# Optimization experiments

Hardware: AMD Instinct MI355X
Metric: run time of the kernel (lower is better)

Reference implementation:

```python
import jax, jax.numpy as jnp
import numpy as np

EMBED = 1024
HEADS = 16


def setup_inputs() -> dict:
    key = jax.random.key(0)
    ks = jax.random.split(key, 7)
    scale = 1.0 / np.sqrt(EMBED)
    x = jax.random.normal(ks[0], (4, 2048, EMBED), dtype=jnp.float32)
    Wq = jax.random.normal(ks[1], (EMBED, EMBED), dtype=jnp.float32) * scale
    bq = jax.random.normal(ks[2], (EMBED,), dtype=jnp.float32) * 0.01
    Wk = jax.random.normal(ks[3], (EMBED, EMBED), dtype=jnp.float32) * scale
    bk = jax.random.normal(ks[4], (EMBED,), dtype=jnp.float32) * 0.01
    Wv = jax.random.normal(ks[5], (EMBED, EMBED), dtype=jnp.float32) * scale
    bv = jax.random.normal(ks[6], (EMBED,), dtype=jnp.float32) * 0.01
    return {"x": x, "Wq": Wq, "bq": bq, "Wk": Wk, "bk": bk, "Wv": Wv, "bv": bv}


def reference(x, Wq, bq, Wk, bk, Wv, bv):
    b, s, n = x.shape
    h = HEADS
    d = n // h
    # torch nn.Linear: y = x @ W.T + b
    q = (jnp.einsum("bsn,mn->bsm", x, Wq) + bq).reshape(b, s, h, d).transpose(0, 2, 1, 3)
    k = (jnp.einsum("bsn,mn->bsm", x, Wk) + bk).reshape(b, s, h, d).transpose(0, 2, 1, 3)
    v = (jnp.einsum("bsn,mn->bsm", x, Wv) + bv).reshape(b, s, h, d).transpose(0, 2, 1, 3)
    # scores: [b, h, s_q, s_k]; fixed scale of 1/10 as in the source
    scores = jnp.einsum("bhqd,bhkd->bhqk", q, k) / 10.0
    # NOTE: softmax over dim=-2 (the QUERY axis), matching the source exactly
    attn = jax.nn.softmax(scores, axis=-2)
    out = jnp.einsum("bhqk,bhkd->bhqd", attn, v)
    return out.transpose(0, 2, 1, 3).reshape(b, s, n)
```

## Files before the change

kernel.cpp:

```cpp
#include <hip/hip_runtime.h>
#include <math.h>

#define SEQ    2048
#define EMBED  1024
#define HEADS  16
#define HDIM   64
#define BATCH  4
#define ROWS   (BATCH * SEQ)
#define BH     (BATCH * HEADS)

typedef _Float16 f16;
typedef __attribute__((ext_vector_type(2))) _Float16 f16x2;
typedef __attribute__((ext_vector_type(4))) _Float16 f16x4;
typedef __attribute__((ext_vector_type(8))) _Float16 f16x8;
typedef __attribute__((ext_vector_type(4)))  float   f32x4;
typedef __attribute__((ext_vector_type(16))) float   f32x16;

#define EXP2C 0.14426950408889634f

__device__ __forceinline__ void async16(void* l, const void* g) {
    __builtin_amdgcn_global_load_lds(
        (__attribute__((address_space(1))) void*)(uintptr_t)g,
        (__attribute__((address_space(3))) void*)(uint32_t)(uintptr_t)l,
        16, 0, 0);
}
__device__ __forceinline__ f32x4 mfma16(f16x8 a, f16x8 b, f32x4 c) {
    return __builtin_amdgcn_mfma_f32_16x16x32_f16(a, b, c, 0, 0, 0);
}
__device__ __forceinline__ f32x16 mfma32(f16x8 a, f16x8 b, f32x16 c) {
    return __builtin_amdgcn_mfma_f32_32x32x16_f16(a, b, c, 0, 0, 0);
}
__device__ __forceinline__ f32x16 zero16() {
    f32x16 z;
#pragma unroll
    for (int i = 0; i < 16; ++i) z[i] = 0.f;
    return z;
}
__device__ __forceinline__ f16x2 pk2(float a, float b) {
    union {
        __fp16 __attribute__((ext_vector_type(2))) h;
        f16x2 f;
    } u;
    u.h = __builtin_amdgcn_cvt_pkrtz(a, b);
    return u.f;
}
__device__ __forceinline__ int swz64(int row, int gran) {
    return row * 64 + ((gran ^ (row & 7)) << 3);
}

#define NX4 (ROWS * EMBED / 4)
#define NW4 (EMBED * EMBED / 4)
__global__ __launch_bounds__(256) void cvt_kernel(
    const float* __restrict__ x,
    const float* __restrict__ Wq, const float* __restrict__ Wk,
    const float* __restrict__ Wv,
    f16* __restrict__ xh, f16* __restrict__ Wh)
{
    int i = blockIdx.x * 256 + threadIdx.x;
    const float4* src; f16* dst; int j;
    if (i < NX4)              { src = (const float4*)x;  dst = xh;                j = i; }
    else if (i < NX4 + NW4)   { src = (const float4*)Wq; dst = Wh;                j = i - NX4; }
    else if (i < NX4 + 2*NW4) { src = (const float4*)Wk; dst = Wh + EMBED*EMBED;  j = i - NX4 - NW4; }
    else                      { src = (const float4*)Wv; dst = Wh + 2*EMBED*EMBED;j = i - NX4 - 2*NW4; }
    float4 v = src[j];
    f16x4 h;
    h[0] = (f16)v.x; h[1] = (f16)v.y; h[2] = (f16)v.z; h[3] = (f16)v.w;
    *(f16x4*)(dst + (size_t)j * 4) = h;
}

__global__ __launch_bounds__(256) void proj_kernel(
    const f16* __restrict__ A,
    const f16* __restrict__ W,
    const float* __restrict__ bq, const float* __restrict__ bk,
    const float* __restrict__ bv,
    f16* __restrict__ Qh, f16* __restrict__ Kh, f16* __restrict__ Vt)
{
    __shared__ f16 As[128 * 32];
    __shared__ f16 Bs[128 * 32];
    __shared__ f16 Ts[64 * 132];

    const int t = threadIdx.x, wv = t >> 6, lane = t & 63;
    const int lm = lane & 15, quad = lane >> 4;
    const int r0 = blockIdx.x * 128, c0 = blockIdx.y * 128;
    const int wm = wv & 1, wn = wv >> 1;

    const int srow = lane >> 2;
    const int sgr  = (lane & 3) ^ (srow & 3);
    const f16* gA = A + (size_t)(r0 + wv * 32 + srow) * EMBED + sgr * 8;
    const f16* gB = W + (size_t)(c0 + wv * 32 + srow) * EMBED + sgr * 8;
    f16* lA = As + wv * 1024;
    f16* lB = Bs + wv * 1024;

    f32x4 acc[4][4];
#pragma unroll
    for (int i = 0; i < 4; ++i)
#pragma unroll
        for (int j = 0; j < 4; ++j) acc[i][j] = (f32x4){0.f, 0.f, 0.f, 0.f};

    for (int kk = 0; kk < EMBED; kk += 32) {
        __syncthreads();
        async16(lA,        gA + kk);
        async16(lA + 512,  gA + (size_t)16 * EMBED + kk);
        async16(lB,        gB + kk);
        async16(lB + 512,  gB + (size_t)16 * EMBED + kk);
        __syncthreads();

        f16x8 af[4], bf[4];
#pragma unroll
        for (int i = 0; i < 4; ++i) {
            int row = wm * 64 + i * 16 + lm;
            af[i] = *(const f16x8*)&As[row * 32 + ((quad ^ (row & 3)) << 3)];
        }
#pragma unroll
        for (int i = 0; i < 4; ++i) {
            int row = wn * 64 + i * 16 + lm;
            bf[i] = *(const f16x8*)&Bs[row * 32 + ((quad ^ (row & 3)) << 3)];
        }
#pragma unroll
        for (int mi = 0; mi < 4; ++mi)
#pragma unroll
            for (int ni = 0; ni < 4; ++ni)
                acc[mi][ni] = mfma16(af[mi], bf[ni], acc[mi][ni]);
    }

    const int z = c0 >> 10;
    const float* bias = (z == 0) ? bq : (z == 1) ? bk : bv;
    const int b  = r0 >> 11;
    const int s0 = r0 & 2047;

    if (z < 2) {
        f16* O = (z == 0) ? Qh : Kh;
#pragma unroll
        for (int ni = 0; ni < 4; ++ni) {
            int cz = (c0 & 1023) + wn * 64 + ni * 16 + lm;
            float bb = bias[cz];
            int h = cz >> 6, d = cz & 63;
#pragma unroll
            for (int mi = 0; mi < 4; ++mi) {
                int s = s0 + wm * 64 + mi * 16 + quad * 4;
                size_t base = ((size_t)(b * HEADS + h) * SEQ + s) * HDIM + d;
#pragma unroll
                for (int r = 0; r < 4; ++r)
                    O[base + (size_t)r * HDIM] = (f16)(acc[mi][ni][r] + bb);
            }
        }
    } else {
#pragma unroll 1
        for (int hd = 0; hd < 2; ++hd) {
            __syncthreads();
            if (wn == hd) {
#pragma unroll
                for (int ni = 0; ni < 4; ++ni) {
                    int cz = (c0 & 1023) + wn * 64 + ni * 16 + lm;
                    float bb = bias[cz];
                    int dloc = ni * 16 + lm;
#pragma unroll
                    for (int mi = 0; mi < 4; ++mi) {
                        int sloc = wm * 64 + mi * 16 + quad * 4;
                        f16x4 pk;
#pragma unroll
                        for (int r = 0; r < 4; ++r) pk[r] = (f16)(acc[mi][ni][r] + bb);
                        *(f16x4*)&Ts[dloc * 132 + sloc] = pk;
                    }
                }
            }
            __syncthreads();
            int hout = ((c0 & 1023) >> 6) + hd;
            int dl = t >> 2, soff = (t & 3) * 32;
            size_t gbase = ((size_t)(b * HEADS + hout) * HDIM + dl) * SEQ + s0 + soff;
#pragma unroll
            for (int c = 0; c < 8; ++c) {
                f16x4 v = *(const f16x4*)&Ts[dl * 132 + soff + 4 * c];
                *(f16x4*)&Vt[gbase + 4 * c] = v;
            }
        }
    }
}

__global__ __launch_bounds__(256) void stats_kernel(
    const f16* __restrict__ Qh, const f16* __restrict__ Kh,
    f16* __restrict__ Vt)
{
    __shared__ f16 Kst[256 * 64];
    __shared__ f16 Qs[64 * 64];
    __shared__ f16 Ls[256];

    const int t = threadIdx.x, wv = t >> 6, lane = t & 63;
    const int lm = lane & 31, half = lane >> 5;
    const int bh = blockIdx.y, k0 = blockIdx.x * 256;
    const size_t base  = (size_t)bh * SEQ * HDIM;
    const size_t vbase = (size_t)bh * HDIM * SEQ;

    const int srow = lane >> 3;
    const int sgr  = (lane & 7) ^ (srow & 7);

#pragma unroll
    for (int i = 0; i < 8; ++i) {
        int rr = wv * 64 + 8 * i;
        async16(Kst + rr * 64,
                Kh + base + (size_t)(k0 + rr + srow) * 64 + sgr * 8);
    }
    __syncthreads();

    f16x8 Kf[2][4];
#pragma unroll
    for (int kt = 0; kt < 2; ++kt)
#pragma unroll
        for (int kg = 0; kg < 4; ++kg)
            Kf[kt][kg] = *(const f16x8*)&Kst[swz64(wv * 64 + kt * 32 + lm, 2 * kg + half)];

    float cs0 = 0.f, cs1 = 0.f;
    for (int q0 = 0; q0 < SEQ; q0 += 64) {
        __syncthreads();
#pragma unroll
        for (int i = 0; i < 2; ++i) {
            int rr = wv * 16 + 8 * i;
            async16(Qs + rr * 64,
                    Qh + base + (size_t)(q0 + rr + srow) * 64 + sgr * 8);
        }
        __syncthreads();
#pragma unroll
        for (int qt = 0; qt < 2; ++qt) {
            f16x8 Qf[4];
#pragma unroll
            for (int kg = 0; kg < 4; ++kg)
                Qf[kg] = *(const f16x8*)&Qs[swz64(qt * 32 + lm, 2 * kg + half)];
            f32x16 s0v = zero16(), s1v = zero16();
#pragma unroll
            for (int kg = 0; kg < 4; ++kg) {
                s0v = mfma32(Qf[kg], Kf[0][kg], s0v);
                s1v = mfma32(Qf[kg], Kf[1][kg], s1v);
            }
#pragma unroll
            for (int e = 0; e < 16; ++e) {
                cs0 += exp2f(s0v[e] * EXP2C);
                cs1 += exp2f(s1v[e] * EXP2C);
            }
        }
    }
    cs0 += __shfl_xor(cs0, 32, 64);
    cs1 += __shfl_xor(cs1, 32, 64);
    if (half == 0) {
        Ls[wv * 64 + lm]      = (f16)(64.0f / cs0);
        Ls[wv * 64 + 32 + lm] = (f16)(64.0f / cs1);
    }
    __syncthreads();

    {
        int dl = t >> 2, koff = (t & 3) * 64;
        size_t g = vbase + (size_t)dl * SEQ + k0 + koff;
#pragma unroll
        for (int c = 0; c < 8; ++c) {
            f16x8 v  = *(const f16x8*)&Vt[g + 8 * c];
            f16x8 lv = *(const f16x8*)&Ls[koff + 8 * c];
            v = v * lv;
            *(f16x8*)&Vt[g + 8 * c] = v;
        }
    }
}

__global__ __launch_bounds__(256) void out_kernel(
    const f16* __restrict__ Qh, const f16* __restrict__ Kh,
    const f16* __restrict__ Vt, float* __restrict__ out)
{
    __shared__ f16 Qs[256 * 64];
    __shared__ f16 Ks[64 * 64];
    __shared__ f16 Vs[64 * 64];

    const int t = threadIdx.x, wv = t >> 6, lane = t & 63;
    const int lm = lane & 31, half = lane >> 5;
    const int bh = blockIdx.y, q0 = blockIdx.x * 256;
    const int b = bh >> 4, h = bh & 15;
    const size_t base  = (size_t)bh * SEQ * HDIM;
    const size_t vbase = (size_t)bh * HDIM * SEQ;

    const int srow = lane >> 3;
    const int sgr  = (lane & 7) ^ (srow & 7);

#pragma unroll
    for (int i = 0; i < 8; ++i) {
        int rr = wv * 64 + 8 * i;
        async16(Qs + rr * 64,
                Qh + base + (size_t)(q0 + rr + srow) * 64 + sgr * 8);
    }
    __syncthreads();

    f16x8 Qf[2][4];
#pragma unroll
    for (int qt = 0; qt < 2; ++qt)
#pragma unroll
        for (int kg = 0; kg < 4; ++kg)
            Qf[qt][kg] = *(const f16x8*)&Qs[swz64(wv * 64 + qt * 32 + lm, 2 * kg + half)];

    f32x16 oacc[2][2];
#pragma unroll
    for (int i = 0; i < 2; ++i)
#pragma unroll
        for (int j = 0; j < 2; ++j) oacc[i][j] = zero16();

    f16* Pw = Qs + wv * 64 * 64;

    for (int k0 = 0; k0 < SEQ; k0 += 64) {
        __syncthreads();
#pragma unroll
        for (int i = 0; i < 2; ++i) {
            int rr = wv * 16 + 8 * i;
            async16(Ks + rr * 64,
                    Kh + base + (size_t)(k0 + rr + srow) * 64 + sgr * 8);
            async16(Vs + rr * 64,
                    Vt + vbase + (size_t)(rr + srow) * SEQ + k0 + sgr * 8);
        }
        __syncthreads();

#pragma unroll
        for (int kt = 0; kt < 2; ++kt) {
            f16x8 Kfr[4];
#pragma unroll
            for (int kg = 0; kg < 4; ++kg)
                Kfr[kg] = *(const f16x8*)&Ks[swz64(kt * 32 + lm, 2 * kg + half)];
#pragma unroll
            for (int qt = 0; qt < 2; ++qt) {
                f32x16 st = zero16();
#pragma unroll
                for (int kg = 0; kg < 4; ++kg)
                    st = mfma32(Kfr[kg], Qf[qt][kg], st);
                int row = qt * 32 + lm;
#pragma unroll
                for (int g = 0; g < 4; ++g) {
                    union { f16x2 h2[2]; f16x4 h4; } u;
                    u.h2[0] = pk2(exp2f(st[4*g+0] * EXP2C), exp2f(st[4*g+1] * EXP2C));
                    u.h2[1] = pk2(exp2f(st[4*g+2] * EXP2C), exp2f(st[4*g+3] * EXP2C));
                    *(f16x4*)&Pw[row * 64 + (((4*kt+g) ^ (row & 7)) << 3) + half * 4] = u.h4;
                }
            }
        }

        f16x8 Vf[2][4];
#pragma unroll
        for (int dt = 0; dt < 2; ++dt)
#pragma unroll
            for (int kc = 0; kc < 4; ++kc)
                Vf[dt][kc] = *(const f16x8*)&Vs[swz64(dt * 32 + lm, 2 * kc + half)];
#pragma unroll
        for (int qt = 0; qt < 2; ++qt) {
            int row = qt * 32 + lm;
#pragma unroll
            for (int kc = 0; kc < 4; ++kc) {
                f16x8 Pf = *(const f16x8*)&Pw[row * 64 + (((2*kc+half) ^ (row & 7)) << 3)];
                oacc[qt][0] = mfma32(Pf, Vf[0][kc], oacc[qt][0]);
                oacc[qt][1] = mfma32(Pf, Vf[1][kc], oacc[qt][1]);
            }
        }
    }

#pragma unroll
    for (int qt = 0; qt < 2; ++qt)
#pragma unroll
        for (int dt = 0; dt < 2; ++dt) {
            int col = h * HDIM + dt * 32 + lm;
#pragma unroll
            for (int e = 0; e < 16; ++e) {
                int s = q0 + wv * 64 + qt * 32 + (e & 3) + 8 * (e >> 2) + 4 * half;
                out[((size_t)b * SEQ + s) * EMBED + col] = oacc[qt][dt][e] * 0.015625f;
            }
        }
}

extern "C" void kernel_launch(void* const* d_in, const int* in_sizes, int n_in,
                              void* d_out, int out_size, void* d_ws, size_t ws_size,
                              hipStream_t stream) {
    const float* x  = (const float*)d_in[0];
    const float* Wq = (const float*)d_in[1];
    const float* bq = (const float*)d_in[2];
    const float* Wk = (const float*)d_in[3];
    const float* bk = (const float*)d_in[4];
    const float* Wv = (const float*)d_in[5];
    const float* bv = (const float*)d_in[6];
    float* out = (float*)d_out;

    f16* xh = (f16*)d_ws;
    f16* Wh = xh + (size_t)ROWS * EMBED;
    f16* Qh = Wh + (size_t)3 * EMBED * EMBED;
    f16* Kh = Qh + (size_t)BH * SEQ * HDIM;
    f16* Vt = Kh + (size_t)BH * SEQ * HDIM;

    cvt_kernel<<<(NX4 + 3 * NW4) / 256, 256, 0, stream>>>(x, Wq, Wk, Wv, xh, Wh);
    proj_kernel<<<dim3(ROWS / 128, 3 * EMBED / 128), 256, 0, stream>>>(
        xh, Wh, bq, bk, bv, Qh, Kh, Vt);
    stats_kernel<<<dim3(SEQ / 256, BH), 256, 0, stream>>>(Qh, Kh, Vt);
    out_kernel<<<dim3(SEQ / 256, BH), 256, 0, stream>>>(Qh, Kh, Vt, out);
}
```

Measured before the change: 370.2 us.

## Double-buffer projection GEMM, fold exp2 scale into Q, halve attention tiles

```diff
diff --git a/kernel.cpp b/kernel.cpp
--- a/kernel.cpp
+++ b/kernel.cpp
@@ -75,8 +75,8 @@
     const float* __restrict__ bv,
     f16* __restrict__ Qh, f16* __restrict__ Kh, f16* __restrict__ Vt)
 {
-    __shared__ f16 As[128 * 32];
-    __shared__ f16 Bs[128 * 32];
+    __shared__ f16 Asb[2][4096];
+    __shared__ f16 Bsb[2][4096];
     __shared__ f16 Ts[64 * 132];
 
     const int t = threadIdx.x, wv = t >> 6, lane = t & 63;
@@ -88,8 +88,6 @@
     const int sgr  = (lane & 3) ^ (srow & 3);
     const f16* gA = A + (size_t)(r0 + wv * 32 + srow) * EMBED + sgr * 8;
     const f16* gB = W + (size_t)(c0 + wv * 32 + srow) * EMBED + sgr * 8;
-    f16* lA = As + wv * 1024;
-    f16* lB = Bs + wv * 1024;
 
     f32x4 acc[4][4];
 #pragma unroll
@@ -97,30 +95,38 @@
 #pragma unroll
         for (int j = 0; j < 4; ++j) acc[i][j] = (f32x4){0.f, 0.f, 0.f, 0.f};
 
-    for (int kk = 0; kk < EMBED; kk += 32) {
-        __syncthreads();
-        async16(lA,        gA + kk);
-        async16(lA + 512,  gA + (size_t)16 * EMBED + kk);
-        async16(lB,        gB + kk);
-        async16(lB + 512,  gB + (size_t)16 * EMBED + kk);
-        __syncthreads();
-
+    async16(&Asb[0][wv * 1024],       gA);
+    async16(&Asb[0][wv * 1024 + 512], gA + (size_t)16 * EMBED);
+    async16(&Bsb[0][wv * 1024],       gB);
+    async16(&Bsb[0][wv * 1024 + 512], gB + (size_t)16 * EMBED);
+    __syncthreads();
+
+    for (int it = 0; it < 32; ++it) {
+        const int cur = it & 1;
+        if (it + 1 < 32) {
+            const int kk = (it + 1) * 32;
+            async16(&Asb[cur ^ 1][wv * 1024],       gA + kk);
+            async16(&Asb[cur ^ 1][wv * 1024 + 512], gA + (size_t)16 * EMBED + kk);
+            async16(&Bsb[cur ^ 1][wv * 1024],       gB + kk);
+            async16(&Bsb[cur ^ 1][wv * 1024 + 512], gB + (size_t)16 * EMBED + kk);
+        }
         f16x8 af[4], bf[4];
 #pragma unroll
         for (int i = 0; i < 4; ++i) {
             int row = wm * 64 + i * 16 + lm;
-            af[i] = *(const f16x8*)&As[row * 32 + ((quad ^ (row & 3)) << 3)];
+            af[i] = *(const f16x8*)&Asb[cur][row * 32 + ((quad ^ (row & 3)) << 3)];
         }
 #pragma unroll
         for (int i = 0; i < 4; ++i) {
             int row = wn * 64 + i * 16 + lm;
-            bf[i] = *(const f16x8*)&Bs[row * 32 + ((quad ^ (row & 3)) << 3)];
+            bf[i] = *(const f16x8*)&Bsb[cur][row * 32 + ((quad ^ (row & 3)) << 3)];
         }
 #pragma unroll
         for (int mi = 0; mi < 4; ++mi)
 #pragma unroll
             for (int ni = 0; ni < 4; ++ni)
                 acc[mi][ni] = mfma16(af[mi], bf[ni], acc[mi][ni]);
+        __syncthreads();
     }
 
     const int z = c0 >> 10;
@@ -130,6 +136,7 @@
 
     if (z < 2) {
         f16* O = (z == 0) ? Qh : Kh;
+        const float scl = (z == 0) ? EXP2C : 1.0f;
 #pragma unroll
         for (int ni = 0; ni < 4; ++ni) {
             int cz = (c0 & 1023) + wn * 64 + ni * 16 + lm;
@@ -141,7 +148,7 @@
                 size_t base = ((size_t)(b * HEADS + h) * SEQ + s) * HDIM + d;
 #pragma unroll
                 for (int r = 0; r < 4; ++r)
-                    O[base + (size_t)r * HDIM] = (f16)(acc[mi][ni][r] + bb);
+                    O[base + (size_t)r * HDIM] = (f16)((acc[mi][ni][r] + bb) * scl);
             }
         }
     } else {
@@ -181,13 +188,13 @@
     const f16* __restrict__ Qh, const f16* __restrict__ Kh,
     f16* __restrict__ Vt)
 {
-    __shared__ f16 Kst[256 * 64];
+    __shared__ f16 Kst[128 * 64];
     __shared__ f16 Qs[64 * 64];
-    __shared__ f16 Ls[256];
+    __shared__ f16 Ls[128];
 
     const int t = threadIdx.x, wv = t >> 6, lane = t & 63;
     const int lm = lane & 31, half = lane >> 5;
-    const int bh = blockIdx.y, k0 = blockIdx.x * 256;
+    const int bh = blockIdx.y, k0 = blockIdx.x * 128;
     const size_t base  = (size_t)bh * SEQ * HDIM;
     const size_t vbase = (size_t)bh * HDIM * SEQ;
 
@@ -195,21 +202,19 @@
     const int sgr  = (lane & 7) ^ (srow & 7);
 
 #pragma unroll
-    for (int i = 0; i < 8; ++i) {
-        int rr = wv * 64 + 8 * i;
+    for (int i = 0; i < 4; ++i) {
+        int rr = wv * 32 + 8 * i;
         async16(Kst + rr * 64,
                 Kh + base + (size_t)(k0 + rr + srow) * 64 + sgr * 8);
     }
     __syncthreads();
 
-    f16x8 Kf[2][4];
-#pragma unroll
-    for (int kt = 0; kt < 2; ++kt)
-#pragma unroll
-        for (int kg = 0; kg < 4; ++kg)
-            Kf[kt][kg] = *(const f16x8*)&Kst[swz64(wv * 64 + kt * 32 + lm, 2 * kg + half)];
-
-    float cs0 = 0.f, cs1 = 0.f;
+    f16x8 Kf[4];
+#pragma unroll
+    for (int kg = 0; kg < 4; ++kg)
+        Kf[kg] = *(const f16x8*)&Kst[swz64(wv * 32 + lm, 2 * kg + half)];
+
+    float cs = 0.f;
     for (int q0 = 0; q0 < SEQ; q0 += 64) {
         __syncthreads();
 #pragma unroll
@@ -225,32 +230,25 @@
 #pragma unroll
             for (int kg = 0; kg < 4; ++kg)
                 Qf[kg] = *(const f16x8*)&Qs[swz64(qt * 32 + lm, 2 * kg + half)];
-            f32x16 s0v = zero16(), s1v = zero16();
-#pragma unroll
-            for (int kg = 0; kg < 4; ++kg) {
-                s0v = mfma32(Qf[kg], Kf[0][kg], s0v);
-                s1v = mfma32(Qf[kg], Kf[1][kg], s1v);
-            }
-#pragma unroll
-            for (int e = 0; e < 16; ++e) {
-                cs0 += exp2f(s0v[e] * EXP2C);
-                cs1 += exp2f(s1v[e] * EXP2C);
-            }
-        }
-    }
-    cs0 += __shfl_xor(cs0, 32, 64);
-    cs1 += __shfl_xor(cs1, 32, 64);
-    if (half == 0) {
-        Ls[wv * 64 + lm]      = (f16)(64.0f / cs0);
-        Ls[wv * 64 + 32 + lm] = (f16)(64.0f / cs1);
-    }
+            f32x16 sv = zero16();
+#pragma unroll
+            for (int kg = 0; kg < 4; ++kg)
+                sv = mfma32(Qf[kg], Kf[kg], sv);
+#pragma unroll
+            for (int e = 0; e < 16; ++e)
+                cs += exp2f(sv[e]);
+        }
+    }
+    cs += __shfl_xor(cs, 32, 64);
+    if (half == 0)
+        Ls[wv * 32 + lm] = (f16)(64.0f / cs);
     __syncthreads();
 
     {
-        int dl = t >> 2, koff = (t & 3) * 64;
+        int dl = t >> 2, koff = (t & 3) * 32;
         size_t g = vbase + (size_t)dl * SEQ + k0 + koff;
 #pragma unroll
-        for (int c = 0; c < 8; ++c) {
+        for (int c = 0; c < 4; ++c) {
             f16x8 v  = *(const f16x8*)&Vt[g + 8 * c];
             f16x8 lv = *(const f16x8*)&Ls[koff + 8 * c];
             v = v * lv;
@@ -263,13 +261,13 @@
     const f16* __restrict__ Qh, const f16* __restrict__ Kh,
     const f16* __restrict__ Vt, float* __restrict__ out)
 {
-    __shared__ f16 Qs[256 * 64];
+    __shared__ f16 Qs[128 * 64];
     __shared__ f16 Ks[64 * 64];
     __shared__ f16 Vs[64 * 64];
 
     const int t = threadIdx.x, wv = t >> 6, lane = t & 63;
     const int lm = lane & 31, half = lane >> 5;
-    const int bh = blockIdx.y, q0 = blockIdx.x * 256;
+    const int bh = blockIdx.y, q0 = blockIdx.x * 128;
     const int b = bh >> 4, h = bh & 15;
     const size_t base  = (size_t)bh * SEQ * HDIM;
     const size_t vbase = (size_t)bh * HDIM * SEQ;
@@ -278,29 +276,25 @@
     const int sgr  = (lane & 7) ^ (srow & 7);
 
 #pragma unroll
-    for (int i = 0; i < 8; ++i) {
-        int rr = wv * 64 + 8 * i;
+    for (int i = 0; i < 4; ++i) {
+        int rr = wv * 32 + 8 * i;
         async16(Qs + rr * 64,
                 Qh + base + (size_t)(q0 + rr + srow) * 64 + sgr * 8);
     }
     __syncthreads();
 
-    f16x8 Qf[2][4];
-#pragma unroll
-    for (int qt = 0; qt < 2; ++qt)
-#pragma unroll
-        for (int kg = 0; kg < 4; ++kg)
-            Qf[qt][kg] = *(const f16x8*)&Qs[swz64(wv * 64 + qt * 32 + lm, 2 * kg + half)];
-
-    f32x16 oacc[2][2];
-#pragma unroll
-    for (int i = 0; i < 2; ++i)
-#pragma unroll
-        for (int j = 0; j < 2; ++j) oacc[i][j] = zero16();
-
-    f16* Pw = Qs + wv * 64 * 64;
-
-    for (int k0 = 0; k0 < SEQ; k0 += 64) {
+    f16x8 Qf[4];
+#pragma unroll
+    for (int kg = 0; kg < 4; ++kg)
+        Qf[kg] = *(const f16x8*)&Qs[swz64(wv * 32 + lm, 2 * kg + half)];
+
+    f32x16 oacc[2];
+    oacc[0] = zero16(); oacc[1] = zero16();
+
+    f16* Pw = Qs + wv * 32 * 64;
+
+    for (int it = 0; it < 32; ++it) {
+        const int k0 = it * 64;
         __syncthreads();
 #pragma unroll
         for (int i = 0; i < 2; ++i) {
@@ -318,52 +312,39 @@
 #pragma unroll
             for (int kg = 0; kg < 4; ++kg)
                 Kfr[kg] = *(const f16x8*)&Ks[swz64(kt * 32 + lm, 2 * kg + half)];
-#pragma unroll
-            for (int qt = 0; qt < 2; ++qt) {
-                f32x16 st = zero16();
-#pragma unroll
-                for (int kg = 0; kg < 4; ++kg)
-                    st = mfma32(Kfr[kg], Qf[qt][kg], st);
-                int row = qt * 32 + lm;
-#pragma unroll
-                for (int g = 0; g < 4; ++g) {
-                    union { f16x2 h2[2]; f16x4 h4; } u;
-                    u.h2[0] = pk2(exp2f(st[4*g+0] * EXP2C), exp2f(st[4*g+1] * EXP2C));
-                    u.h2[1] = pk2(exp2f(st[4*g+2] * EXP2C), exp2f(st[4*g+3] * EXP2C));
-                    *(f16x4*)&Pw[row * 64 + (((4*kt+g) ^ (row & 7)) << 3) + half * 4] = u.h4;
-                }
+            f32x16 st = zero16();
+#pragma unroll
+            for (int kg = 0; kg < 4; ++kg)
+                st = mfma32(Kfr[kg], Qf[kg], st);
+            const int row = lm;
+#pragma unroll
+            for (int g = 0; g < 4; ++g) {
+                union { f16x2 h2[2]; f16x4 h4; } u;
+                u.h2[0] = pk2(exp2f(st[4*g+0]), exp2f(st[4*g+1]));
+                u.h2[1] = pk2(exp2f(st[4*g+2]), exp2f(st[4*g+3]));
+                *(f16x4*)&Pw[row * 64 + (((4*kt+g) ^ (row & 7)) << 3) + half * 4] = u.h4;
             }
         }
 
-        f16x8 Vf[2][4];
-#pragma unroll
-        for (int dt = 0; dt < 2; ++dt)
-#pragma unroll
-            for (int kc = 0; kc < 4; ++kc)
-                Vf[dt][kc] = *(const f16x8*)&Vs[swz64(dt * 32 + lm, 2 * kc + half)];
-#pragma unroll
-        for (int qt = 0; qt < 2; ++qt) {
-            int row = qt * 32 + lm;
-#pragma unroll
-            for (int kc = 0; kc < 4; ++kc) {
-                f16x8 Pf = *(const f16x8*)&Pw[row * 64 + (((2*kc+half) ^ (row & 7)) << 3)];
-                oacc[qt][0] = mfma32(Pf, Vf[0][kc], oacc[qt][0]);
-                oacc[qt][1] = mfma32(Pf, Vf[1][kc], oacc[qt][1]);
-            }
-        }
-    }
-
-#pragma unroll
-    for (int qt = 0; qt < 2; ++qt)
-#pragma unroll
-        for (int dt = 0; dt < 2; ++dt) {
-            int col = h * HDIM + dt * 32 + lm;
-#pragma unroll
-            for (int e = 0; e < 16; ++e) {
-                int s = q0 + wv * 64 + qt * 32 + (e & 3) + 8 * (e >> 2) + 4 * half;
-                out[((size_t)b * SEQ + s) * EMBED + col] = oacc[qt][dt][e] * 0.015625f;
-            }
-        }
+#pragma unroll
+        for (int kc = 0; kc < 4; ++kc) {
+            f16x8 Pf  = *(const f16x8*)&Pw[lm * 64 + (((2*kc+half) ^ (lm & 7)) << 3)];
+            f16x8 Vf0 = *(const f16x8*)&Vs[swz64(lm,      2 * kc + half)];
+            f16x8 Vf1 = *(const f16x8*)&Vs[swz64(32 + lm, 2 * kc + half)];
+            oacc[0] = mfma32(Pf, Vf0, oacc[0]);
+            oacc[1] = mfma32(Pf, Vf1, oacc[1]);
+        }
+    }
+
+#pragma unroll
+    for (int dt = 0; dt < 2; ++dt) {
+        int col = h * HDIM + dt * 32 + lm;
+#pragma unroll
+        for (int e = 0; e < 16; ++e) {
+            int s = q0 + wv * 32 + (e & 3) + 8 * (e >> 2) + 4 * half;
+            out[((size_t)b * SEQ + s) * EMBED + col] = oacc[dt][e] * 0.015625f;
+        }
+    }
 }
 
 extern "C" void kernel_launch(void* const* d_in, const int* in_sizes, int n_in,
@@ -387,6 +368,6 @@
     cvt_kernel<<<(NX4 + 3 * NW4) / 256, 256, 0, stream>>>(x, Wq, Wk, Wv, xh, Wh);
     proj_kernel<<<dim3(ROWS / 128, 3 * EMBED / 128), 256, 0, stream>>>(
         xh, Wh, bq, bk, bv, Qh, Kh, Vt);
-    stats_kernel<<<dim3(SEQ / 256, BH), 256, 0, stream>>>(Qh, Kh, Vt);
-    out_kernel<<<dim3(SEQ / 256, BH), 256, 0, stream>>>(Qh, Kh, Vt, out);
-}
+    stats_kernel<<<dim3(SEQ / 128, BH), 256, 0, stream>>>(Qh, Kh, Vt);
+    out_kernel<<<dim3(SEQ / 128, BH), 256, 0, stream>>>(Qh, Kh, Vt, out);
+}
```

After: 358.1 us. -3.3%, faster.
